# Kernel optimization log

Hardware: AMD Instinct MI355X
Metric: run time of the kernel (lower is better)

Reference implementation:

```python
import jax, jax.numpy as jnp
import numpy as np

N, H, V, MAX_STEPS = 256, 128, 64, 4

def setup_inputs() -> dict:
    key = jax.random.key(0)
    ks = jax.random.split(key, 16)
    def w(k, shape, fan_in):
        return jax.random.normal(k, shape, dtype=jnp.float32) / np.sqrt(fan_in)
    inp = {}
    inp['node_embeddings'] = jax.random.normal(ks[0], (N, H), dtype=jnp.float32)
    inp['skip_embeddings'] = jax.random.normal(ks[1], (N, N, H), dtype=jnp.float32)
    inp['Wx'] = w(ks[2], (H, 4 * H), H)
    inp['Wh'] = w(ks[3], (H, 4 * H), H)
    inp['b'] = jnp.zeros((4 * H,), jnp.float32)
    inp['Wxs'] = w(ks[4], (H, 4 * H), H)
    inp['Whs'] = w(ks[5], (H, 4 * H), H)
    inp['bs'] = jnp.zeros((4 * H,), jnp.float32)
    inp['Wb'] = w(ks[6], (2 * H, 2), 2 * H)
    inp['bb'] = jnp.zeros((2,), jnp.float32)
    inp['Wk'] = w(ks[7], (H, H), H)
    inp['bk'] = jnp.zeros((H,), jnp.float32)
    inp['Wq'] = w(ks[8], (2 * H, H), 2 * H)
    inp['bq'] = jnp.zeros((H,), jnp.float32)
    inp['Wl'] = w(ks[9], (2 * H, 1), 2 * H)
    inp['bl'] = jnp.zeros((1,), jnp.float32)
    inp['Wd'] = w(ks[10], (2 * H, V), 2 * H)
    inp['bd'] = jnp.zeros((V,), jnp.float32)
    # valid skips only forward in the program (include diagonal = no-skip)
    inp['skip_mask'] = jnp.triu(jnp.ones((N, N), dtype=bool))
    inp['true_indexes'] = jax.random.randint(ks[11], (N,), 0, N, dtype=jnp.int32)
    inp['false_indexes'] = jax.random.randint(ks[12], (N,), 0, N, dtype=jnp.int32)
    inp['exit_index'] = N - 1
    return inp

def _lstm(c, h, x, Wx, Wh, b):
    gates = x @ Wx + h @ Wh + b  # [..., 4H]
    i, f, g, o = jnp.split(gates, 4, axis=-1)
    c2 = jax.nn.sigmoid(f) * c + jax.nn.sigmoid(i) * jnp.tanh(g)
    h2 = jax.nn.sigmoid(o) * jnp.tanh(c2)
    return c2, h2

def reference(node_embeddings, skip_embeddings, Wx, Wh, b, Wxs, Whs, bs,
              Wb, bb, Wk, bk, Wq, bq, Wl, bl, Wd, bd,
              skip_mask, true_indexes, false_indexes, exit_index):
    n, hdim = node_embeddings.shape
    eye = jnp.eye(n, dtype=node_embeddings.dtype)
    ip0 = jnp.zeros((n,), node_embeddings.dtype).at[0].set(1.0)
    c0 = jnp.zeros((n, hdim), node_embeddings.dtype)
    h0 = jnp.zeros((n, hdim), node_embeddings.dtype)
    keys = skip_embeddings @ Wk + bk  # [N,N,H] (input-only, precompute)

    def step(carry, _):
        ip, c, h = carry
        # per-node LSTM proposals
        c_p, h_p = _lstm(c, h, node_embeddings, Wx, Wh, b)  # [N,H]
        hid = jnp.concatenate([c_p, h_p], axis=-1)  # [N,2H]
        # skip proposals: carry of source i applied to skip embedding (i,j)
        c_sk, h_sk = _lstm(c[:, None, :], h[:, None, :], skip_embeddings, Wxs, Whs, bs)  # [N,N,H]
        # branch decisions
        branch = jax.nn.softmax(hid @ Wb + bb, axis=-1)  # [N,2]
        # skip decisions (per source i, softmax over destinations j)
        queries = hid @ Wq + bq  # [N,H]
        kq = jax.nn.relu(jnp.concatenate(
            [keys, jnp.broadcast_to(queries[:, None, :], (n, n, hdim))], axis=-1))  # [N,N,2H]
        logits = jnp.einsum('ijk,kl->ijl', kq, Wl)[..., 0] + bl[0]  # [N,N]
        skip_dec = jax.nn.softmax(jnp.where(skip_mask, logits, -jnp.inf), axis=-1)
        # aggregation (IPA)
        yes_skip = skip_dec * (1.0 - eye)  # zero diagonal
        no_skip = jnp.diagonal(skip_dec)
        p_bt = ip * no_skip * branch[:, 0]
        p_bf = ip * no_skip * branch[:, 1]
        new_ip = (jax.ops.segment_sum(p_bt, true_indexes, num_segments=n)
                  + jax.ops.segment_sum(p_bf, false_indexes, num_segments=n)
                  + jnp.einsum('i,ij->j', ip, yes_skip))
        denom = new_ip[:, None] + 1e-7
        def agg(hp, hsk):
            t = jax.ops.segment_sum(hp * p_bt[:, None], true_indexes, num_segments=n)
            f = jax.ops.segment_sum(hp * p_bf[:, None], false_indexes, num_segments=n)
            s = jnp.einsum('ijh,i,ij->jh', hsk, ip, yes_skip)
            return (t + f + s) / denom
        return (new_ip, agg(c_p, c_sk), agg(h_p, h_sk)), None

    (ip, c, h), _ = jax.lax.scan(step, (ip0, c0, h0), None, length=MAX_STEPS)
    exit_concat = jnp.concatenate([c[exit_index], h[exit_index]], axis=-1)  # [2H]
    return exit_concat @ Wd + bd  # [V]
```

## Files before the change

kernel.cpp:

```cpp
#include <hip/hip_runtime.h>
#include <hip/hip_bf16.h>

constexpr int NN = 256;
constexpr int HH = 128;
constexpr int GG = 512;
constexpr int NP = NN * NN;
constexpr int NCH = 8;
constexpr int CHSZ = 32;

typedef __attribute__((ext_vector_type(8))) short short8;
typedef __attribute__((ext_vector_type(4))) float f32x4;

__device__ unsigned short g_xs[(size_t)NP * GG];
__device__ unsigned short g_wfr[20 * 512 * 8];
__device__ float g_bsp[GG];
__device__ float g_pwh[HH * HH * 4];
__device__ float g_pws[HH * HH * 4];
__device__ float g_kterm[NP];
__device__ float g_yeswT[NP];
__device__ float g_noskip[NN];
__device__ float g_xg[NN * HH * 4];
__device__ float g_xga[NN * HH * 4];
__device__ float g_hws[NN * HH * 4];
__device__ float g_c[NN * HH];
__device__ float g_h[NN * HH];
__device__ float g_sc[NN * HH];
__device__ float g_sh[NN * HH];
__device__ float g_pc[NCH * NN * HH];
__device__ float g_ph[NCH * NN * HH];
__device__ float g_pw[NCH * NN];
__device__ float g_ip[NN];
__device__ float g_nip[NN];

__device__ __forceinline__ unsigned short f2bf(float f) {
  unsigned int u = __float_as_uint(f);
  u = (u + 0x7fffu + ((u >> 16) & 1u)) >> 16;
  return (unsigned short)u;
}
__device__ __forceinline__ float bf2f(unsigned short s) {
  return __uint_as_float(((unsigned int)s) << 16);
}
__device__ __forceinline__ float frcp(float x) {
#if __has_builtin(__builtin_amdgcn_rcpf)
  return __builtin_amdgcn_rcpf(x);
#else
  return 1.0f / x;
#endif
}
__device__ __forceinline__ float sigm(float x) { return frcp(1.f + __expf(-x)); }
__device__ __forceinline__ float tanhfast(float x) { return 1.f - 2.f * frcp(__expf(2.f * x) + 1.f); }

__global__ __launch_bounds__(512) void k_pre(const float* __restrict__ NE,
                                             const float* __restrict__ Wx,
                                             const float* __restrict__ b,
                                             const float* __restrict__ Wxs,
                                             const float* __restrict__ Wk,
                                             const float* __restrict__ bs,
                                             const float* __restrict__ Wh,
                                             const float* __restrict__ Whs) {
  const int bid = blockIdx.x;
  const int tid = threadIdx.x;
  if (bid < 64) {
    const int idx = bid * 512 + tid;
    g_sc[idx] = 0.f; g_sh[idx] = 0.f; g_c[idx] = 0.f; g_h[idx] = 0.f;
    *(float4*)&g_hws[(size_t)idx * 4] = make_float4(0.f, 0.f, 0.f, 0.f);
    if (idx < NN) { g_nip[idx] = 0.f; g_ip[idx] = (idx == 0) ? 1.f : 0.f; }
  } else if (bid < 84) {
    const int bidx = bid - 64;
    const int tile = bidx >> 2, ks = bidx & 3;
    const int ct = tid >> 6, l = tid & 63;
    const int c = ct * 16 + (l & 15);
    const int kbase = ks * 32 + (l >> 4) * 8;
    int src = 0;
    if (tile < 4) src = (c & 3) * 128 + tile * 32 + (c >> 2);
    unsigned short* dst = &g_wfr[((size_t)bidx * 512 + tid) * 8];
#pragma unroll
    for (int e = 0; e < 8; ++e) {
      int k = kbase + e;
      float v = (tile < 4) ? Wxs[k * GG + src] : Wk[k * HH + c];
      dst[e] = f2bf(v);
    }
    if (tile < 4 && ks == 0 && (l >> 4) == 0) g_bsp[tile * 128 + c] = bs[src];
  } else if (bid < 116) {
    const int k = (bid - 84) * 4 + (tid >> 7), t = tid & 127;
    float4 a = make_float4(Wh[k * GG + t], Wh[k * GG + 128 + t], Wh[k * GG + 256 + t], Wh[k * GG + 384 + t]);
    float4 s = make_float4(Whs[k * GG + t], Whs[k * GG + 128 + t], Whs[k * GG + 256 + t], Whs[k * GG + 384 + t]);
    *(float4*)&g_pwh[((size_t)k * HH + t) * 4] = a;
    *(float4*)&g_pws[((size_t)k * HH + t) * 4] = s;
  } else {
    __shared__ float ne[4][HH];
    const int sub = tid >> 7, t = tid & 127;
    const int i = (bid - 116) * 4 + sub;
    ne[sub][t] = NE[i * HH + t];
    __syncthreads();
    float a0 = b[t], a1 = b[128 + t], a2 = b[256 + t], a3 = b[384 + t];
    for (int k = 0; k < HH; ++k) {
      float x = ne[sub][k];
      a0 = fmaf(x, Wx[k * GG + t], a0);
      a1 = fmaf(x, Wx[k * GG + 128 + t], a1);
      a2 = fmaf(x, Wx[k * GG + 256 + t], a2);
      a3 = fmaf(x, Wx[k * GG + 384 + t], a3);
    }
    float4 v = make_float4(a0, a1, a2, a3);
    *(float4*)&g_xg[((size_t)i * HH + t) * 4] = v;
    *(float4*)&g_xga[((size_t)i * HH + t) * 4] = v;
  }
}

__device__ __forceinline__ void loadB(short8* dst, int tile, int ks, int l) {
  const unsigned short* wf = &g_wfr[((size_t)(tile * 4 + ks)) * 4096 + l * 8];
#pragma unroll
  for (int ct = 0; ct < 8; ++ct) dst[ct] = *(const short8*)(wf + ct * 512);
}

__global__ __launch_bounds__(256) void k_gemm(const float* __restrict__ SE,
                                              const float* __restrict__ bk,
                                              const float* __restrict__ Wl) {
  __shared__ __align__(16) char lds[32768];
  const int bid = blockIdx.x;
  const int tile = blockIdx.y;
  const int pb = (bid < 128) ? (bid * 2) : ((bid - 128) * 2 + 1);
  const int pairBase = pb * 128;
  const int tid = threadIdx.x;

  for (int cc = tid; cc < 2048; cc += 256) {
    int row = cc >> 4, kc = cc & 15;
    const float* src = SE + (size_t)(pairBase + row) * HH + kc * 8;
    float4 f0 = *(const float4*)(src);
    float4 f1 = *(const float4*)(src + 4);
    short8 v;
    v[0] = (short)f2bf(f0.x); v[1] = (short)f2bf(f0.y); v[2] = (short)f2bf(f0.z); v[3] = (short)f2bf(f0.w);
    v[4] = (short)f2bf(f1.x); v[5] = (short)f2bf(f1.y); v[6] = (short)f2bf(f1.z); v[7] = (short)f2bf(f1.w);
    *(short8*)(lds + row * 256 + ((kc * 16) ^ ((row & 7) << 4))) = v;
  }
  __syncthreads();

  const int wv = tid >> 6;
  const int l = tid & 63;
  const int l15 = l & 15, lg = l >> 4;

  f32x4 acc[2][8];
#pragma unroll
  for (int rt = 0; rt < 2; ++rt)
#pragma unroll
    for (int ct = 0; ct < 8; ++ct) acc[rt][ct] = (f32x4){0.f, 0.f, 0.f, 0.f};

  short8 bA[8], bB[8];
  loadB(bA, tile, 0, l);
#pragma unroll
  for (int ks = 0; ks < 4; ks += 2) {
    loadB(bB, tile, ks + 1, l);
    {
      const int kb = ks * 64 + lg * 16;
      short8 a[2];
#pragma unroll
      for (int rt = 0; rt < 2; ++rt) {
        int row = wv * 32 + rt * 16 + l15;
        a[rt] = *(const short8*)(lds + row * 256 + (kb ^ ((row & 7) << 4)));
      }
#pragma unroll
      for (int rt = 0; rt < 2; ++rt)
#pragma unroll
        for (int ct = 0; ct < 8; ++ct)
          acc[rt][ct] = __builtin_amdgcn_mfma_f32_16x16x32_bf16(a[rt], bA[ct], acc[rt][ct], 0, 0, 0);
    }
    if (ks + 2 < 4) loadB(bA, tile, ks + 2, l);
    {
      const int kb = (ks + 1) * 64 + lg * 16;
      short8 a[2];
#pragma unroll
      for (int rt = 0; rt < 2; ++rt) {
        int row = wv * 32 + rt * 16 + l15;
        a[rt] = *(const short8*)(lds + row * 256 + (kb ^ ((row & 7) << 4)));
      }
#pragma unroll
      for (int rt = 0; rt < 2; ++rt)
#pragma unroll
        for (int ct = 0; ct < 8; ++ct)
          acc[rt][ct] = __builtin_amdgcn_mfma_f32_16x16x32_bf16(a[rt], bB[ct], acc[rt][ct], 0, 0, 0);
    }
  }

  if (tile < 4) {
#pragma unroll
    for (int rt = 0; rt < 2; ++rt)
#pragma unroll
      for (int ct = 0; ct < 8; ++ct) {
        const int col = ct * 16 + l15;
        const float bsv = g_bsp[tile * 128 + col];
#pragma unroll
        for (int r = 0; r < 4; ++r) {
          int row = wv * 32 + rt * 16 + lg * 4 + r;
          int pair = pairBase + row;
          int jj = pair & 255, ii = pair >> 8;
          if (jj > ii)
            g_xs[((size_t)jj * NN + ii) * GG + tile * 128 + col] = f2bf(acc[rt][ct][r] + bsv);
        }
      }
  } else {
#pragma unroll
    for (int rt = 0; rt < 2; ++rt) {
#pragma unroll
      for (int r = 0; r < 4; ++r) {
        float s = 0.f;
#pragma unroll
        for (int ct = 0; ct < 8; ++ct) {
          int col = ct * 16 + l15;
          float x = acc[rt][ct][r] + bk[col];
          x = fmaxf(x, 0.f);
          s = fmaf(x, Wl[col], s);
        }
#pragma unroll
        for (int m = 1; m < 16; m <<= 1) s += __shfl_xor(s, m, 64);
        int row = wv * 32 + rt * 16 + lg * 4 + r;
        int pair = pairBase + row;
        int jj = pair & 255, ii = pair >> 8;
        if (l15 == 0 && jj >= ii) g_kterm[pair] = s;
      }
    }
  }
}

__global__ __launch_bounds__(256) void k_softmax() {
  const int i = blockIdx.x, j = threadIdx.x;
  __shared__ float sm[NN];
  float x = -1e30f;
  if (j >= i) x = g_kterm[i * NN + j];
  sm[j] = x;
  __syncthreads();
  for (int s = 128; s > 0; s >>= 1) { if (j < s) sm[j] = fmaxf(sm[j], sm[j + s]); __syncthreads(); }
  float mx = sm[0];
  __syncthreads();
  float e = (j >= i) ? __expf(x - mx) : 0.f;
  sm[j] = e;
  __syncthreads();
  for (int s = 128; s > 0; s >>= 1) { if (j < s) sm[j] += sm[j + s]; __syncthreads(); }
  float p = e * frcp(sm[0]);
  g_yeswT[j * NN + i] = (j == i) ? 0.f : p;
  if (j == i) g_noskip[i] = p;
}

__global__ __launch_bounds__(128) void k_step(const float* __restrict__ Wb,
                                              const float* __restrict__ bb,
                                              const int* __restrict__ tix,
                                              const int* __restrict__ fix) {
  const int t = threadIdx.x;
  if (blockIdx.x < 256) {
    const int i = blockIdx.x;
    __shared__ float red[2][2];
    const float4 a = *(const float4*)&g_xga[((size_t)i * HH + t) * 4];
    float co = g_c[i * HH + t];
    float c2 = sigm(a.y) * co + sigm(a.x) * tanhfast(a.z);
    float h2 = sigm(a.w) * tanhfast(c2);
    float q0 = c2 * Wb[2 * t] + h2 * Wb[2 * (128 + t)];
    float q1 = c2 * Wb[2 * t + 1] + h2 * Wb[2 * (128 + t) + 1];
#pragma unroll
    for (int m = 1; m < 64; m <<= 1) { q0 += __shfl_xor(q0, m, 64); q1 += __shfl_xor(q1, m, 64); }
    if ((t & 63) == 0) { red[t >> 6][0] = q0; red[t >> 6][1] = q1; }
    __syncthreads();
    float l0 = red[0][0] + red[1][0] + bb[0];
    float l1 = red[0][1] + red[1][1] + bb[1];
    float mm = fmaxf(l0, l1);
    float e0 = __expf(l0 - mm), e1 = __expf(l1 - mm);
    float inv = frcp(e0 + e1);
    float ipv = g_ip[i] * g_noskip[i];
    if (ipv != 0.f) {
      float pbt = ipv * e0 * inv, pbf = ipv * e1 * inv;
      int ti = tix[i], fi = fix[i];
      atomicAdd(&g_sc[ti * HH + t], c2 * pbt);
      atomicAdd(&g_sh[ti * HH + t], h2 * pbt);
      atomicAdd(&g_sc[fi * HH + t], c2 * pbf);
      atomicAdd(&g_sh[fi * HH + t], h2 * pbf);
      if (t == 0) { atomicAdd(&g_nip[ti], pbt); atomicAdd(&g_nip[fi], pbf); }
    }
  } else {
    const int idx = blockIdx.x - 256;
    const int j = idx >> 3, ch = idx & 7;
    const int i0 = ch * CHSZ;
    if (i0 >= j) return;
    const int iN = (j - i0 < CHSZ) ? (j - i0) : CHSZ;
    __shared__ float wsh[CHSZ];
    if (t < CHSZ) wsh[t] = (t < iN) ? g_ip[i0 + t] * g_yeswT[j * NN + i0 + t] : 0.f;
    __syncthreads();
    float accC = 0.f, accH = 0.f, accW = 0.f;
    for (int ii = 0; ii < iN; ++ii) {
      float wgt = wsh[ii];
      if (wgt == 0.f) continue;
      const int i = i0 + ii;
      const ushort4 gv = *(const ushort4*)&g_xs[((size_t)j * NN + i) * GG + t * 4];
      float4 hw = *(const float4*)&g_hws[((size_t)i * HH + t) * 4];
      float xi = bf2f(gv.x) + hw.x;
      float xf = bf2f(gv.y) + hw.y;
      float xg = bf2f(gv.z) + hw.z;
      float xo = bf2f(gv.w) + hw.w;
      float c2 = sigm(xf) * g_c[i * HH + t] + sigm(xi) * tanhfast(xg);
      float h2 = sigm(xo) * tanhfast(c2);
      accC = fmaf(wgt, c2, accC);
      accH = fmaf(wgt, h2, accH);
      accW += wgt;
    }
    g_pc[((size_t)ch * NN + j) * HH + t] = accC;
    g_ph[((size_t)ch * NN + j) * HH + t] = accH;
    if (t == 0) g_pw[ch * NN + j] = accW;
  }
}

__global__ __launch_bounds__(256) void k_finish(const int last) {
  const int j0 = blockIdx.x * 4;
  const int tid = threadIdx.x;
  __shared__ float hsm[4][HH];
  __shared__ float nipsh[4];
  if (tid < 4) {
    const int j = j0 + tid;
    float nip = g_nip[j];
    const int nch = (j + 31) >> 5;
    for (int ch = 0; ch < nch; ++ch) nip += g_pw[ch * NN + j];
    nipsh[tid] = nip;
    g_ip[j] = nip;
    g_nip[j] = 0.f;
  }
  __syncthreads();
#pragma unroll
  for (int s = 0; s < 2; ++s) {
    const int slot = tid + s * 256;
    const int jj = slot >> 7, t = slot & 127;
    const int j = j0 + jj;
    float sc = g_sc[j * HH + t], sh = g_sh[j * HH + t];
    const int nch = (j + 31) >> 5;
    for (int ch = 0; ch < nch; ++ch) {
      sc += g_pc[((size_t)ch * NN + j) * HH + t];
      sh += g_ph[((size_t)ch * NN + j) * HH + t];
    }
    float d = frcp(nipsh[jj] + 1e-7f);
    float cv = sc * d, hv = sh * d;
    g_c[j * HH + t] = cv;
    g_h[j * HH + t] = hv;
    hsm[jj][t] = hv;
    g_sc[j * HH + t] = 0.f;
    g_sh[j * HH + t] = 0.f;
  }
  __syncthreads();
  if (last) return;
  const int m = tid >> 7, t = tid & 127;
  const float* __restrict__ W = m ? g_pws : g_pwh;
  float4 a0 = make_float4(0.f, 0.f, 0.f, 0.f), a1 = a0, a2 = a0, a3 = a0;
#pragma unroll 4
  for (int k = 0; k < HH; ++k) {
    const float4 w = *(const float4*)&W[((size_t)k * HH + t) * 4];
    const float h0 = hsm[0][k], h1 = hsm[1][k], h2 = hsm[2][k], h3 = hsm[3][k];
    a0.x = fmaf(h0, w.x, a0.x); a0.y = fmaf(h0, w.y, a0.y); a0.z = fmaf(h0, w.z, a0.z); a0.w = fmaf(h0, w.w, a0.w);
    a1.x = fmaf(h1, w.x, a1.x); a1.y = fmaf(h1, w.y, a1.y); a1.z = fmaf(h1, w.z, a1.z); a1.w = fmaf(h1, w.w, a1.w);
    a2.x = fmaf(h2, w.x, a2.x); a2.y = fmaf(h2, w.y, a2.y); a2.z = fmaf(h2, w.z, a2.z); a2.w = fmaf(h2, w.w, a2.w);
    a3.x = fmaf(h3, w.x, a3.x); a3.y = fmaf(h3, w.y, a3.y); a3.z = fmaf(h3, w.z, a3.z); a3.w = fmaf(h3, w.w, a3.w);
  }
  if (m == 0) {
    float4 x0 = *(const float4*)&g_xg[((size_t)(j0 + 0) * HH + t) * 4];
    float4 x1 = *(const float4*)&g_xg[((size_t)(j0 + 1) * HH + t) * 4];
    float4 x2 = *(const float4*)&g_xg[((size_t)(j0 + 2) * HH + t) * 4];
    float4 x3 = *(const float4*)&g_xg[((size_t)(j0 + 3) * HH + t) * 4];
    *(float4*)&g_xga[((size_t)(j0 + 0) * HH + t) * 4] = make_float4(x0.x + a0.x, x0.y + a0.y, x0.z + a0.z, x0.w + a0.w);
    *(float4*)&g_xga[((size_t)(j0 + 1) * HH + t) * 4] = make_float4(x1.x + a1.x, x1.y + a1.y, x1.z + a1.z, x1.w + a1.w);
    *(float4*)&g_xga[((size_t)(j0 + 2) * HH + t) * 4] = make_float4(x2.x + a2.x, x2.y + a2.y, x2.z + a2.z, x2.w + a2.w);
    *(float4*)&g_xga[((size_t)(j0 + 3) * HH + t) * 4] = make_float4(x3.x + a3.x, x3.y + a3.y, x3.z + a3.z, x3.w + a3.w);
  } else {
    *(float4*)&g_hws[((size_t)(j0 + 0) * HH + t) * 4] = a0;
    *(float4*)&g_hws[((size_t)(j0 + 1) * HH + t) * 4] = a1;
    *(float4*)&g_hws[((size_t)(j0 + 2) * HH + t) * 4] = a2;
    *(float4*)&g_hws[((size_t)(j0 + 3) * HH + t) * 4] = a3;
  }
}

__global__ __launch_bounds__(64) void k_out(const float* __restrict__ Wd,
                                            const float* __restrict__ bd,
                                            const int* __restrict__ ei,
                                            float* __restrict__ out) {
  const int v = threadIdx.x;
  const int e = ei[0];
  float s = bd[v];
  for (int h = 0; h < HH; ++h) {
    s = fmaf(g_c[e * HH + h], Wd[h * 64 + v], s);
    s = fmaf(g_h[e * HH + h], Wd[(128 + h) * 64 + v], s);
  }
  out[v] = s;
}

extern "C" void kernel_launch(void* const* d_in, const int* in_sizes, int n_in,
                              void* d_out, int out_size, void* d_ws, size_t ws_size,
                              hipStream_t stream) {
  const float* NE  = (const float*)d_in[0];
  const float* SE  = (const float*)d_in[1];
  const float* Wx  = (const float*)d_in[2];
  const float* Wh  = (const float*)d_in[3];
  const float* b   = (const float*)d_in[4];
  const float* Wxs = (const float*)d_in[5];
  const float* Whs = (const float*)d_in[6];
  const float* bs  = (const float*)d_in[7];
  const float* Wb  = (const float*)d_in[8];
  const float* bb  = (const float*)d_in[9];
  const float* Wk  = (const float*)d_in[10];
  const float* bk  = (const float*)d_in[11];
  const float* Wl  = (const float*)d_in[14];
  const float* Wd  = (const float*)d_in[16];
  const float* bd  = (const float*)d_in[17];
  const int* tix = (const int*)d_in[19];
  const int* fix = (const int*)d_in[20];
  const int* ei  = (const int*)d_in[21];
  float* out = (float*)d_out;

  k_pre<<<180, 512, 0, stream>>>(NE, Wx, b, Wxs, Wk, bs, Wh, Whs);
  k_gemm<<<dim3(384, 5), 256, 0, stream>>>(SE, bk, Wl);
  k_softmax<<<256, 256, 0, stream>>>();
  for (int s = 0; s < 4; ++s) {
    k_step<<<256 + NN * NCH, 128, 0, stream>>>(Wb, bb, tix, fix);
    k_finish<<<64, 256, 0, stream>>>(s == 3);
  }
  k_out<<<1, 64, 0, stream>>>(Wd, bd, ei, out);
}
```

Measured before the change: 179.7 us.

## Skip inactive nodes, reduce skip partials via atomics, remap gemm grid per XCD, fuse output

k_step now returns early for nodes whose instruction-pointer mass is zero and for whole 16-wide skip chunks whose weights are all zero. The per-chunk partial buffers and their reduction in k_finish are replaced by direct atomicAdd into the shared accumulators. The gemm grid is flattened and remapped so consecutive blocks land on the same XCD, and the final output projection is folded into the last k_finish launch. Atomics add contention and make the summation order nondeterministic.

```diff
diff --git a/kernel.cpp b/kernel.cpp
--- a/kernel.cpp
+++ b/kernel.cpp
@@ -5,8 +5,6 @@
 constexpr int HH = 128;
 constexpr int GG = 512;
 constexpr int NP = NN * NN;
-constexpr int NCH = 8;
-constexpr int CHSZ = 32;
 
 typedef __attribute__((ext_vector_type(8))) short short8;
 typedef __attribute__((ext_vector_type(4))) float f32x4;
@@ -14,21 +12,18 @@
 __device__ unsigned short g_xs[(size_t)NP * GG];
 __device__ unsigned short g_wfr[20 * 512 * 8];
 __device__ float g_bsp[GG];
-__device__ float g_pwh[HH * HH * 4];
-__device__ float g_pws[HH * HH * 4];
+__device__ float g_pwh[HH * GG];
+__device__ float g_pws[HH * GG];
 __device__ float g_kterm[NP];
 __device__ float g_yeswT[NP];
 __device__ float g_noskip[NN];
-__device__ float g_xg[NN * HH * 4];
-__device__ float g_xga[NN * HH * 4];
-__device__ float g_hws[NN * HH * 4];
+__device__ float g_xg[NN * GG];
+__device__ float g_xga[NN * GG];
+__device__ float g_hws[NN * GG];
 __device__ float g_c[NN * HH];
 __device__ float g_h[NN * HH];
 __device__ float g_sc[NN * HH];
 __device__ float g_sh[NN * HH];
-__device__ float g_pc[NCH * NN * HH];
-__device__ float g_ph[NCH * NN * HH];
-__device__ float g_pw[NCH * NN];
 __device__ float g_ip[NN];
 __device__ float g_nip[NN];
 
@@ -118,8 +113,11 @@
                                               const float* __restrict__ Wl) {
   __shared__ __align__(16) char lds[32768];
   const int bid = blockIdx.x;
-  const int tile = blockIdx.y;
-  const int pb = (bid < 128) ? (bid * 2) : ((bid - 128) * 2 + 1);
+  const int xcd = bid & 7;
+  const int w = bid >> 3;
+  const int x = (w / 5) * 8 + xcd;
+  const int tile = w % 5;
+  const int pb = (x < 128) ? (x * 2) : ((x - 128) * 2 + 1);
   const int pairBase = pb * 128;
   const int tid = threadIdx.x;
 
@@ -206,9 +204,9 @@
 #pragma unroll
         for (int ct = 0; ct < 8; ++ct) {
           int col = ct * 16 + l15;
-          float x = acc[rt][ct][r] + bk[col];
-          x = fmaxf(x, 0.f);
-          s = fmaf(x, Wl[col], s);
+          float x2 = acc[rt][ct][r] + bk[col];
+          x2 = fmaxf(x2, 0.f);
+          s = fmaf(x2, Wl[col], s);
         }
 #pragma unroll
         for (int m = 1; m < 16; m <<= 1) s += __shfl_xor(s, m, 64);
@@ -247,6 +245,8 @@
   const int t = threadIdx.x;
   if (blockIdx.x < 256) {
     const int i = blockIdx.x;
+    const float ipi = g_ip[i];
+    if (ipi == 0.f) return;
     __shared__ float red[2][2];
     const float4 a = *(const float4*)&g_xga[((size_t)i * HH + t) * 4];
     float co = g_c[i * HH + t];
@@ -263,7 +263,7 @@
     float mm = fmaxf(l0, l1);
     float e0 = __expf(l0 - mm), e1 = __expf(l1 - mm);
     float inv = frcp(e0 + e1);
-    float ipv = g_ip[i] * g_noskip[i];
+    float ipv = ipi * g_noskip[i];
     if (ipv != 0.f) {
       float pbt = ipv * e0 * inv, pbf = ipv * e1 * inv;
       int ti = tix[i], fi = fix[i];
@@ -275,17 +275,20 @@
     }
   } else {
     const int idx = blockIdx.x - 256;
-    const int j = idx >> 3, ch = idx & 7;
-    const int i0 = ch * CHSZ;
+    const int j = idx >> 4, ch = idx & 15;
+    const int i0 = ch * 16;
     if (i0 >= j) return;
-    const int iN = (j - i0 < CHSZ) ? (j - i0) : CHSZ;
-    __shared__ float wsh[CHSZ];
-    if (t < CHSZ) wsh[t] = (t < iN) ? g_ip[i0 + t] * g_yeswT[j * NN + i0 + t] : 0.f;
+    const int iN = (j - i0 < 16) ? (j - i0) : 16;
+    __shared__ float wsh[16];
+    if (t < 16) wsh[t] = (t < iN) ? g_ip[i0 + t] * g_yeswT[j * NN + i0 + t] : 0.f;
     __syncthreads();
+    float s16 = 0.f;
+#pragma unroll
+    for (int q = 0; q < 16; ++q) s16 += wsh[q];
+    if (s16 == 0.f) return;
     float accC = 0.f, accH = 0.f, accW = 0.f;
     for (int ii = 0; ii < iN; ++ii) {
-      float wgt = wsh[ii];
-      if (wgt == 0.f) continue;
+      const float wgt = wsh[ii];
       const int i = i0 + ii;
       const ushort4 gv = *(const ushort4*)&g_xs[((size_t)j * NN + i) * GG + t * 4];
       float4 hw = *(const float4*)&g_hws[((size_t)i * HH + t) * 4];
@@ -299,13 +302,17 @@
       accH = fmaf(wgt, h2, accH);
       accW += wgt;
     }
-    g_pc[((size_t)ch * NN + j) * HH + t] = accC;
-    g_ph[((size_t)ch * NN + j) * HH + t] = accH;
-    if (t == 0) g_pw[ch * NN + j] = accW;
-  }
-}
-
-__global__ __launch_bounds__(256) void k_finish(const int last) {
+    atomicAdd(&g_sc[j * HH + t], accC);
+    atomicAdd(&g_sh[j * HH + t], accH);
+    if (t == 0) atomicAdd(&g_nip[j], accW);
+  }
+}
+
+__global__ __launch_bounds__(256) void k_finish(const int last,
+                                                const float* __restrict__ Wd,
+                                                const float* __restrict__ bd,
+                                                const int* __restrict__ ei,
+                                                float* __restrict__ out) {
   const int j0 = blockIdx.x * 4;
   const int tid = threadIdx.x;
   __shared__ float hsm[4][HH];
@@ -313,8 +320,6 @@
   if (tid < 4) {
     const int j = j0 + tid;
     float nip = g_nip[j];
-    const int nch = (j + 31) >> 5;
-    for (int ch = 0; ch < nch; ++ch) nip += g_pw[ch * NN + j];
     nipsh[tid] = nip;
     g_ip[j] = nip;
     g_nip[j] = 0.f;
@@ -325,14 +330,9 @@
     const int slot = tid + s * 256;
     const int jj = slot >> 7, t = slot & 127;
     const int j = j0 + jj;
-    float sc = g_sc[j * HH + t], sh = g_sh[j * HH + t];
-    const int nch = (j + 31) >> 5;
-    for (int ch = 0; ch < nch; ++ch) {
-      sc += g_pc[((size_t)ch * NN + j) * HH + t];
-      sh += g_ph[((size_t)ch * NN + j) * HH + t];
-    }
     float d = frcp(nipsh[jj] + 1e-7f);
-    float cv = sc * d, hv = sh * d;
+    float cv = g_sc[j * HH + t] * d;
+    float hv = g_sh[j * HH + t] * d;
     g_c[j * HH + t] = cv;
     g_h[j * HH + t] = hv;
     hsm[jj][t] = hv;
@@ -340,7 +340,21 @@
     g_sh[j * HH + t] = 0.f;
   }
   __syncthreads();
-  if (last) return;
+  if (last) {
+    const int e = ei[0];
+    if (e >= j0 && e < j0 + 4 && tid < 64) {
+      const int v = tid;
+      float sacc = bd[v];
+      const float* cc = &g_c[e * HH];
+      const float* hh = &g_h[e * HH];
+      for (int h = 0; h < HH; ++h) {
+        sacc = fmaf(cc[h], Wd[h * 64 + v], sacc);
+        sacc = fmaf(hh[h], Wd[(128 + h) * 64 + v], sacc);
+      }
+      out[v] = sacc;
+    }
+    return;
+  }
   const int m = tid >> 7, t = tid & 127;
   const float* __restrict__ W = m ? g_pws : g_pwh;
   float4 a0 = make_float4(0.f, 0.f, 0.f, 0.f), a1 = a0, a2 = a0, a3 = a0;
@@ -368,20 +382,6 @@
     *(float4*)&g_hws[((size_t)(j0 + 2) * HH + t) * 4] = a2;
     *(float4*)&g_hws[((size_t)(j0 + 3) * HH + t) * 4] = a3;
   }
-}
-
-__global__ __launch_bounds__(64) void k_out(const float* __restrict__ Wd,
-                                            const float* __restrict__ bd,
-                                            const int* __restrict__ ei,
-                                            float* __restrict__ out) {
-  const int v = threadIdx.x;
-  const int e = ei[0];
-  float s = bd[v];
-  for (int h = 0; h < HH; ++h) {
-    s = fmaf(g_c[e * HH + h], Wd[h * 64 + v], s);
-    s = fmaf(g_h[e * HH + h], Wd[(128 + h) * 64 + v], s);
-  }
-  out[v] = s;
 }
 
 extern "C" void kernel_launch(void* const* d_in, const int* in_sizes, int n_in,
@@ -408,11 +408,10 @@
   float* out = (float*)d_out;
 
   k_pre<<<180, 512, 0, stream>>>(NE, Wx, b, Wxs, Wk, bs, Wh, Whs);
-  k_gemm<<<dim3(384, 5), 256, 0, stream>>>(SE, bk, Wl);
+  k_gemm<<<1920, 256, 0, stream>>>(SE, bk, Wl);
   k_softmax<<<256, 256, 0, stream>>>();
   for (int s = 0; s < 4; ++s) {
-    k_step<<<256 + NN * NCH, 128, 0, stream>>>(Wb, bb, tix, fix);
-    k_finish<<<64, 256, 0, stream>>>(s == 3);
-  }
-  k_out<<<1, 64, 0, stream>>>(Wd, bd, ei, out);
-}
+    k_step<<<256 + NN * 16, 128, 0, stream>>>(Wb, bb, tix, fix);
+    k_finish<<<64, 256, 0, stream>>>(s == 3, Wd, bd, ei, out);
+  }
+}
```

Result: faster. 159.6 us (-11.2%).
